# Kernel optimization log

Hardware: AMD Instinct MI355X
Metric: run time of the kernel (lower is better)

Reference implementation:

```python
import jax, jax.numpy as jnp
import numpy as np

B, L, HEADS, D_HEAD = 2, 2048, 16, 64
D_MODEL = HEADS * D_HEAD            # 1024
D_BI = D_MODEL * 4 // 2             # 2048 (bilinear GLU width)
D_PROJ = D_MODEL * 3 + 2 * D_BI
DEPTH = 0                           # block depth < 2 -> token shift active
NEG_INF = -1e10


def _ln(x, g, b, eps=1e-5):
    m = jnp.mean(x, axis=-1, keepdims=True)
    v = jnp.var(x, axis=-1, keepdims=True)
    return (x - m) * jax.lax.rsqrt(v + eps) * g + b


def _shift(x, n):
    # F.pad(x, (0,0,n,-n)): shift along seq dim by n, zero-fill at front
    return jnp.pad(x, ((0, 0), (n, 0), (0, 0)))[:, : x.shape[1], :]


def setup_inputs() -> dict:
    key = jax.random.key(0)
    ks = jax.random.split(key, 3)
    x = jax.random.normal(ks[0], (B, L, D_MODEL), jnp.float32)
    w_in = jax.random.normal(ks[1], (D_MODEL, D_PROJ), jnp.float32) * (D_MODEL ** -0.5)
    # note: torch init zeros out_proj; we use small random weights so backward is non-trivial
    w_out = jax.random.normal(ks[2], (D_MODEL + D_BI, D_MODEL), jnp.float32) * 0.02
    slopes = jnp.concatenate([2.0 ** jnp.linspace(0.0, -6.0, HEADS // 2),
                              jnp.zeros(HEADS - HEADS // 2)]).astype(jnp.float32)
    return {
        "x": x,
        "in_ln_g": jnp.ones(D_MODEL, jnp.float32), "in_ln_b": jnp.zeros(D_MODEL, jnp.float32),
        "mid_ln_g": jnp.ones(D_PROJ, jnp.float32), "mid_ln_b": jnp.zeros(D_PROJ, jnp.float32),
        "out_ln_g": jnp.ones(D_MODEL, jnp.float32), "out_ln_b": jnp.zeros(D_MODEL, jnp.float32),
        "w_in": w_in, "w_out": w_out, "slopes": slopes,
    }


def reference(x, in_ln_g, in_ln_b, mid_ln_g, mid_ln_b, out_ln_g, out_ln_b, w_in, w_out, slopes):
    b, l, d = x.shape
    x = _ln(x, in_ln_g, in_ln_b)
    if DEPTH < 2:
        x = jnp.concatenate([
            _shift(x[..., : d // 4], 1),
            x[..., d // 4: d - d // 8],
            _shift(x[..., d - d // 8:], 2),
        ], axis=-1)
    h = _ln(x @ w_in, mid_ln_g, mid_ln_b)
    q, k, v, p1, p2 = jnp.split(h, [D_MODEL, 2 * D_MODEL, 3 * D_MODEL, 3 * D_MODEL + D_BI], axis=-1)
    to_heads = lambda t: t.reshape(b, l, HEADS, D_HEAD).transpose(0, 2, 1, 3)  # b h l d
    q, k, v = to_heads(q), to_heads(k), to_heads(v)
    logits = jnp.einsum('bhid,bhjd->bhij', q, k) * (D_HEAD ** -0.5)
    pos = jnp.arange(l)
    alibi = pos[None, None, None, :].astype(logits.dtype) * slopes[None, :, None, None]
    causal = jnp.where(pos[:, None] >= pos[None, :], 0.0, NEG_INF).astype(logits.dtype)
    a = jax.nn.softmax(logits + alibi + causal, axis=-1)
    o = jnp.einsum('bhij,bhjd->bhid', a, v).transpose(0, 2, 1, 3).reshape(b, l, d)
    return _ln(jnp.concatenate([o, p1 * p2], axis=-1) @ w_out, out_ln_g, out_ln_b)
```

## Files before the change

kernel.cpp:

```cpp
#include <hip/hip_runtime.h>

#define B_ 2
#define L_ 2048
#define HEADS_ 16
#define DH_ 64
#define DM_ 1024
#define DBI_ 2048
#define DPROJ_ 7168
#define NTOK (B_*L_)
#define DCAT (DM_ + DBI_)

typedef __bf16 bf16;
typedef __attribute__((ext_vector_type(8))) __bf16 bf16x8;
typedef __attribute__((ext_vector_type(4))) __bf16 bf16x4;
typedef __attribute__((ext_vector_type(4))) float floatx4;

typedef __attribute__((address_space(1))) const void gptr_t;
typedef __attribute__((address_space(3))) void lptr_t;

__device__ __forceinline__ void g2l16(const void* g, void* l) {
    __builtin_amdgcn_global_load_lds((gptr_t*)g, (lptr_t*)l, 16, 0, 0);
}

__global__ __launch_bounds__(256) void transpose_both(const float* __restrict__ w_in,
                                                      const float* __restrict__ w_out,
                                                      bf16* __restrict__ w_inT,
                                                      bf16* __restrict__ w_outT) {
    __shared__ float tile[32][33];
    int l = blockIdx.x;
    const float* in; bf16* outp; int R, C, bx, by;
    if (l < 7168) { in = w_in;  outp = w_inT;  R = DM_;  C = DPROJ_; bx = l % 224; by = l / 224; }
    else { l -= 7168; in = w_out; outp = w_outT; R = DCAT; C = DM_;   bx = l % 32;  by = l / 32; }
    int c0 = bx * 32, r0 = by * 32;
    int x = threadIdx.x & 31, y = threadIdx.x >> 5;
    for (int i = 0; i < 32; i += 8)
        tile[y + i][x] = in[(size_t)(r0 + y + i) * C + (c0 + x)];
    __syncthreads();
    for (int i = 0; i < 32; i += 8)
        outp[(size_t)(c0 + y + i) * R + (r0 + x)] = (bf16)tile[x][y + i];
}

__global__ __launch_bounds__(256) void ln_shift(const float* __restrict__ x,
                                                const float* __restrict__ g,
                                                const float* __restrict__ bb,
                                                bf16* __restrict__ xs) {
    int tok = blockIdx.x;
    int b = tok / L_, l = tok % L_;
    int t = threadIdx.x;
    floatx4 v = *(const floatx4*)(x + (size_t)tok * DM_ + t * 4);
    float s = v[0] + v[1] + v[2] + v[3];
    float s2 = v[0]*v[0] + v[1]*v[1] + v[2]*v[2] + v[3]*v[3];
    __shared__ float red[2][4];
    for (int o = 32; o; o >>= 1) { s += __shfl_xor(s, o); s2 += __shfl_xor(s2, o); }
    int w = t >> 6;
    if ((t & 63) == 0) { red[0][w] = s; red[1][w] = s2; }
    __syncthreads();
    s  = red[0][0] + red[0][1] + red[0][2] + red[0][3];
    s2 = red[1][0] + red[1][1] + red[1][2] + red[1][3];
    float mean = s * (1.f / DM_);
    float var  = s2 * (1.f / DM_) - mean * mean;
    float rstd = rsqrtf(var + 1e-5f);
    int c0 = t * 4;
    floatx4 gg = *(const floatx4*)(g + c0);
    floatx4 bv = *(const floatx4*)(bb + c0);
    bf16x4 y;
    #pragma unroll
    for (int i = 0; i < 4; i++) y[i] = (bf16)((v[i] - mean) * rstd * gg[i] + bv[i]);
    int shift = (c0 < 256) ? 1 : ((c0 >= 896) ? 2 : 0);
    int dl = l + shift;
    if (dl < L_) *(bf16x4*)(xs + ((size_t)b * L_ + dl) * DM_ + c0) = y;
    if (l == 0 && shift) {
        bf16x4 z = {};
        *(bf16x4*)(xs + ((size_t)b * L_ + 0) * DM_ + c0) = z;
        if (shift == 2) *(bf16x4*)(xs + ((size_t)b * L_ + 1) * DM_ + c0) = z;
    }
}

__global__ __launch_bounds__(512, 2) void gemm1_fr(const bf16* __restrict__ A,
                                                   const bf16* __restrict__ Bt,
                                                   bf16* __restrict__ C) {
    const int K = DM_, N = DPROJ_;
    int lin = blockIdx.x;
    int xcd = lin & 7, idx = lin >> 3;
    int mt = (xcd >> 2) * 8 + idx / 7;
    int nt = (xcd & 3) * 7 + idx % 7;
    int m0 = mt * 256, n0 = nt * 256;

    __shared__ bf16 As[2][256 * 64];
    __shared__ bf16 Bs[2][256 * 64];

    int t = threadIdx.x;
    int lane = t & 63;
    int c = lane & 15, quad = lane >> 4;
    int wave = t >> 6;
    int wm = (wave >> 2) * 128;
    int wn = (wave & 3) * 64;

    auto stageA = [&](int k0, int bsel, int h) {
        #pragma unroll
        for (int s = 0; s < 2; s++) {
            int g = h * 1024 + s * 512 + t;
            int row = g >> 3;
            int kc = (g & 7) ^ (row & 7);
            g2l16(A + (size_t)(m0 + row) * K + (k0 + kc * 8), &As[bsel][g * 8]);
        }
    };
    auto stageB = [&](int k0, int bsel, int h) {
        #pragma unroll
        for (int s = 0; s < 2; s++) {
            int g = h * 1024 + s * 512 + t;
            int row = g >> 3;
            int kc = (g & 7) ^ (row & 7);
            g2l16(Bt + (size_t)(n0 + row) * K + (k0 + kc * 8), &Bs[bsel][g * 8]);
        }
    };

    floatx4 acc[8][4] = {};

    stageA(0, 0, 0); stageA(0, 0, 1);
    stageB(0, 0, 0); stageB(0, 0, 1);
    stageB(64, 1, 0); stageB(64, 1, 1);
    asm volatile("s_waitcnt vmcnt(4)" ::: "memory");
    __builtin_amdgcn_s_barrier();
    __builtin_amdgcn_sched_barrier(0);

    const int nT = K / 64;
    for (int tt = 0; tt < nT; ++tt) {
        int cur = tt & 1, nxt = cur ^ 1;
        int k1 = (tt + 1) << 6, k2 = (tt + 2) << 6;
        bool dA = (tt + 1 < nT), dB = (tt + 2 < nT);
        bf16x8 bfr[4][2];
        #pragma unroll
        for (int p = 0; p < 4; p++) {
            if      (p == 0) { if (dA) stageA(k1, nxt, 0); }
            else if (p == 1) { if (dA) stageA(k1, nxt, 1); }
            else if (p == 2) { if (dB) stageB(k2, cur, 0); }
            else             { if (dB) stageB(k2, cur, 1); }
            if (p == 0) {
                #pragma unroll
                for (int j = 0; j < 4; j++)
                    #pragma unroll
                    for (int s = 0; s < 2; s++)
                        bfr[j][s] = *(const bf16x8*)&Bs[cur][(wn + j * 16 + c) * 64
                                                            + (((s * 4 + quad) ^ (c & 7)) * 8)];
            }
            bf16x8 af[2][2];
            #pragma unroll
            for (int ii = 0; ii < 2; ii++)
                #pragma unroll
                for (int s = 0; s < 2; s++)
                    af[ii][s] = *(const bf16x8*)&As[cur][(wm + (p * 2 + ii) * 16 + c) * 64
                                                         + (((s * 4 + quad) ^ (c & 7)) * 8)];
            __builtin_amdgcn_s_setprio(1);
            #pragma unroll
            for (int ii = 0; ii < 2; ii++)
                #pragma unroll
                for (int j = 0; j < 4; j++)
                    #pragma unroll
                    for (int s = 0; s < 2; s++)
                        acc[p * 2 + ii][j] = __builtin_amdgcn_mfma_f32_16x16x32_bf16(
                            af[ii][s], bfr[j][s], acc[p * 2 + ii][j], 0, 0, 0);
            __builtin_amdgcn_s_setprio(0);
        }
        asm volatile("s_waitcnt lgkmcnt(0)" ::: "memory");
        if (dB)      { asm volatile("s_waitcnt vmcnt(4)" ::: "memory"); }
        else if (dA) { asm volatile("s_waitcnt vmcnt(0)" ::: "memory"); }
        if (tt + 1 < nT) __builtin_amdgcn_s_barrier();
        __builtin_amdgcn_sched_barrier(0);
    }

    #pragma unroll
    for (int i = 0; i < 8; i++)
        #pragma unroll
        for (int j = 0; j < 4; j++)
            #pragma unroll
            for (int r = 0; r < 4; r++) {
                int row = m0 + wm + i * 16 + quad * 4 + r;
                int col = n0 + wn + j * 16 + c;
                C[(size_t)row * N + col] = (bf16)acc[i][j][r];
            }
}

__global__ __launch_bounds__(256) void gemm2_sk(const bf16* __restrict__ A,
                                                const bf16* __restrict__ Bt,
                                                float* __restrict__ P) {
    const int ldA = DCAT, N = DM_;
    int m0 = blockIdx.x * 128, n0 = blockIdx.y * 128, kz = blockIdx.z;
    const bf16* Ak = A + kz * 1024;
    const bf16* Btk = Bt + kz * 1024;
    float* C = P + (size_t)kz * NTOK * DM_;
    __shared__ bf16 As[2][128 * 32];
    __shared__ bf16 Bs[2][128 * 32];
    int t = threadIdx.x, lane = t & 63, wave = t >> 6;
    int c = lane & 15, quad = lane >> 4;
    int wm = (wave >> 1) * 64, wn = (wave & 1) * 64;
    auto stage = [&](int k0, int bsel) {
        #pragma unroll
        for (int s = 0; s < 2; s++) {
            int f = s * 256 + t;
            int row = f >> 2, kp = (f & 3) * 8;
            g2l16(Ak + (size_t)(m0 + row) * ldA + k0 + kp, &As[bsel][f * 8]);
            g2l16(Btk + (size_t)(n0 + row) * ldA + k0 + kp, &Bs[bsel][f * 8]);
        }
    };
    floatx4 acc[4][4] = {};
    stage(0, 0);
    int buf = 0;
    for (int k0 = 0; k0 < 1024; k0 += 32) {
        __syncthreads();
        if (k0 + 32 < 1024) stage(k0 + 32, buf ^ 1);
        bf16x8 af[4], bfr[4];
        #pragma unroll
        for (int i = 0; i < 4; i++)
            af[i] = *(const bf16x8*)&As[buf][(wm + i * 16 + c) * 32 + quad * 8];
        #pragma unroll
        for (int j = 0; j < 4; j++)
            bfr[j] = *(const bf16x8*)&Bs[buf][(wn + j * 16 + c) * 32 + quad * 8];
        #pragma unroll
        for (int i = 0; i < 4; i++)
            #pragma unroll
            for (int j = 0; j < 4; j++)
                acc[i][j] = __builtin_amdgcn_mfma_f32_16x16x32_bf16(af[i], bfr[j], acc[i][j], 0, 0, 0);
        buf ^= 1;
    }
    #pragma unroll
    for (int i = 0; i < 4; i++)
        #pragma unroll
        for (int j = 0; j < 4; j++)
            #pragma unroll
            for (int r = 0; r < 4; r++) {
                int row = m0 + wm + i * 16 + quad * 4 + r;
                int col = n0 + wn + j * 16 + c;
                C[(size_t)row * N + col] = acc[i][j][r];
            }
}

__global__ __launch_bounds__(256) void mid_ln_fused(const bf16* __restrict__ h,
                                                    const float* __restrict__ g,
                                                    const float* __restrict__ bb,
                                                    bf16* __restrict__ Qp,
                                                    bf16* __restrict__ Kp,
                                                    bf16* __restrict__ Vn,
                                                    bf16* __restrict__ A2) {
    int tok = blockIdx.x;
    int b = tok >> 11, l = tok & 2047;
    size_t base = (size_t)tok * DPROJ_;
    int t = threadIdx.x;
    float v[28];
    float s = 0.f, s2 = 0.f;
    #pragma unroll
    for (int i = 0; i < 7; i++) {
        bf16x4 r = *(const bf16x4*)(h + base + (size_t)(t + i * 256) * 4);
        #pragma unroll
        for (int k = 0; k < 4; k++) {
            float f = (float)r[k];
            v[i * 4 + k] = f; s += f; s2 += f * f;
        }
    }
    __shared__ float red[2][4];
    for (int o = 32; o; o >>= 1) { s += __shfl_xor(s, o); s2 += __shfl_xor(s2, o); }
    int w = t >> 6;
    if ((t & 63) == 0) { red[0][w] = s; red[1][w] = s2; }
    __syncthreads();
    s  = red[0][0] + red[0][1] + red[0][2] + red[0][3];
    s2 = red[1][0] + red[1][1] + red[1][2] + red[1][3];
    float mean = s * (1.f / DPROJ_);
    float var  = s2 * (1.f / DPROJ_) - mean * mean;
    float rstd = rsqrtf(var + 1e-5f);
    #pragma unroll
    for (int i = 0; i < 7; i++) {
        int C0 = (t + i * 256) * 4;
        floatx4 gg = *(const floatx4*)(g + C0);
        floatx4 bv = *(const floatx4*)(bb + C0);
        #pragma unroll
        for (int k = 0; k < 4; k++)
            v[i * 4 + k] = (v[i * 4 + k] - mean) * rstd * gg[k] + bv[k];
    }
    #pragma unroll
    for (int i = 0; i < 3; i++) {
        int C0 = (t + i * 256) * 4;
        int sec = C0 >> 10, cc = C0 & 1023;
        int hh = cc >> 6, d = cc & 63;
        bf16* dst = (sec == 0) ? Qp : (sec == 1) ? Kp : Vn;
        size_t idx = (((size_t)b * HEADS_ + hh) * L_ + l) * DH_ + d;
        bf16x4 o;
        #pragma unroll
        for (int k = 0; k < 4; k++) o[k] = (bf16)v[i * 4 + k];
        *(bf16x4*)(dst + idx) = o;
    }
    #pragma unroll
    for (int i = 3; i < 5; i++) {
        int off = (t + i * 256) * 4 - 3 * DM_;
        bf16x4 o;
        #pragma unroll
        for (int k = 0; k < 4; k++) o[k] = (bf16)(v[i * 4 + k] * v[(i + 2) * 4 + k]);
        *(bf16x4*)(A2 + (size_t)tok * DCAT + DM_ + off) = o;
    }
}

__global__ __launch_bounds__(256) void vt_pack(const bf16* __restrict__ Vn,
                                               bf16* __restrict__ Vt) {
    __shared__ bf16 tile[32][33];
    int bh = blockIdx.z;
    const bf16* in = Vn + (size_t)bh * L_ * DH_;
    bf16* out = Vt + (size_t)bh * DH_ * L_;
    int l0 = blockIdx.x * 32, d0 = blockIdx.y * 32;
    int x = threadIdx.x & 31, y = threadIdx.x >> 5;
    for (int i = 0; i < 32; i += 8)
        tile[y + i][x] = in[(size_t)(l0 + y + i) * DH_ + d0 + x];
    __syncthreads();
    for (int i = 0; i < 32; i += 8)
        out[(size_t)(d0 + y + i) * L_ + l0 + x] = tile[x][y + i];
}

__global__ __launch_bounds__(256, 4) void attn6(const bf16* __restrict__ Qp,
                                                const bf16* __restrict__ Kp,
                                                const bf16* __restrict__ Vt,
                                                const float* __restrict__ slopes,
                                                bf16* __restrict__ A2) {
    int hd = blockIdx.y, b = blockIdx.z;
    int lin = blockIdx.x + 32 * blockIdx.y + 512 * blockIdx.z;
    int xr = blockIdx.x;
    int qt = ((lin >> 8) & 1) ? (31 - xr) : xr;
    int q0 = qt * 64;
    int t = threadIdx.x, lane = t & 63, wave = t >> 6;
    int quad = lane >> 4, c = lane & 15;
    __shared__ bf16 Ks[2][64 * 64];
    __shared__ bf16 Vs[64 * 64];
    __shared__ bf16 Ps[4][16 * 72];
    int bh = b * HEADS_ + hd;
    const bf16* Qb = Qp + (size_t)bh * L_ * DH_;
    const bf16* Kb = Kp + (size_t)bh * L_ * DH_;
    const bf16* Vb = Vt + (size_t)bh * DH_ * L_;
    const float LOG2E = 1.44269504f;
    float slopeL2 = slopes[hd] * LOG2E;
    const float qscale = 0.125f * LOG2E;

    bf16x8 qf[2];
    int qrow = q0 + wave * 16 + c;
    qf[0] = *(const bf16x8*)(Qb + (size_t)qrow * DH_ + quad * 8);
    qf[1] = *(const bf16x8*)(Qb + (size_t)qrow * DH_ + 32 + quad * 8);
    floatx4 accO[4] = {};
    float lsum[4];
    float mrow[4];
    int i_row0 = q0 + wave * 16 + quad * 4;
    #pragma unroll
    for (int r = 0; r < 4; r++) {
        lsum[r] = 0.f;
        mrow[r] = slopeL2 * (float)(i_row0 + r) + 20.0f;
    }

    int row = t >> 2, kp = (t & 3) * 8;
    auto stageK = [&](int j0, int kb) {
        #pragma unroll
        for (int s = 0; s < 2; s++)
            g2l16(Kb + (size_t)(j0 + row) * DH_ + s * 32 + kp, &Ks[kb][(s * 256 + t) * 8]);
    };
    auto stageV = [&](int j0) {
        #pragma unroll
        for (int s = 0; s < 2; s++)
            g2l16(Vb + (size_t)row * L_ + j0 + s * 32 + kp, &Vs[(s * 256 + t) * 8]);
    };

    bf16* pw = &Ps[wave][0];
    bf16* pwr = pw + (quad * 4) * 72 + c;

    stageK(0, 0);
    asm volatile("s_waitcnt vmcnt(0)" ::: "memory");
    __builtin_amdgcn_s_barrier();
    __builtin_amdgcn_sched_barrier(0);

    int kb = 0;
    for (int j0 = 0; j0 <= q0; j0 += 64) {
        bool dK = (j0 + 64 <= q0);
        stageV(j0);
        if (dK) stageK(j0 + 64, kb ^ 1);

        bool diag = (j0 == q0);
        #pragma unroll
        for (int nt = 0; nt < 4; nt++) {
            floatx4 sacc = {};
            bf16x8 kf0 = *(const bf16x8*)&Ks[kb][(nt * 16 + c) * 32 + quad * 8];
            bf16x8 kf1 = *(const bf16x8*)&Ks[kb][2048 + (nt * 16 + c) * 32 + quad * 8];
            sacc = __builtin_amdgcn_mfma_f32_16x16x32_bf16(qf[0], kf0, sacc, 0, 0, 0);
            sacc = __builtin_amdgcn_mfma_f32_16x16x32_bf16(qf[1], kf1, sacc, 0, 0, 0);
            int j = j0 + nt * 16 + c;
            float aj = slopeL2 * (float)j;
            #pragma unroll
            for (int r = 0; r < 4; r++) {
                float p = exp2f(fmaf(sacc[r], qscale, aj) - mrow[r]);
                if (diag) p = (j <= i_row0 + r) ? p : 0.f;
                lsum[r] += p;
                pwr[r * 72 + nt * 16] = (bf16)p;
            }
        }
        bf16x8 pf0 = *(const bf16x8*)&pw[c * 72 + quad * 8];
        bf16x8 pf1 = *(const bf16x8*)&pw[c * 72 + 32 + quad * 8];

        if (dK) { asm volatile("s_waitcnt vmcnt(2)" ::: "memory"); }
        else    { asm volatile("s_waitcnt vmcnt(0)" ::: "memory"); }
        __builtin_amdgcn_s_barrier();
        __builtin_amdgcn_sched_barrier(0);

        #pragma unroll
        for (int nt = 0; nt < 4; nt++) {
            bf16x8 vf0 = *(const bf16x8*)&Vs[(nt * 16 + c) * 32 + quad * 8];
            bf16x8 vf1 = *(const bf16x8*)&Vs[2048 + (nt * 16 + c) * 32 + quad * 8];
            accO[nt] = __builtin_amdgcn_mfma_f32_16x16x32_bf16(pf0, vf0, accO[nt], 0, 0, 0);
            accO[nt] = __builtin_amdgcn_mfma_f32_16x16x32_bf16(pf1, vf1, accO[nt], 0, 0, 0);
        }
        asm volatile("s_waitcnt lgkmcnt(0)" ::: "memory");
        __builtin_amdgcn_s_barrier();
        __builtin_amdgcn_sched_barrier(0);
        kb ^= 1;
    }
    #pragma unroll
    for (int r = 0; r < 4; r++) {
        float l = lsum[r];
        l += __shfl_xor(l, 1);
        l += __shfl_xor(l, 2);
        l += __shfl_xor(l, 4);
        l += __shfl_xor(l, 8);
        lsum[r] = 1.f / l;
    }
    #pragma unroll
    for (int r = 0; r < 4; r++) {
        size_t orow = (size_t)b * L_ + q0 + wave * 16 + quad * 4 + r;
        #pragma unroll
        for (int nt = 0; nt < 4; nt++)
            A2[orow * DCAT + hd * DH_ + nt * 16 + c] = (bf16)(accO[nt][r] * lsum[r]);
    }
}

__global__ __launch_bounds__(256) void out_ln3(const float* __restrict__ P,
                                               const float* __restrict__ g,
                                               const float* __restrict__ bb,
                                               float* __restrict__ out) {
    size_t base = (size_t)blockIdx.x * DM_;
    const size_t stride = (size_t)NTOK * DM_;
    int t = threadIdx.x;
    floatx4 a = *(const floatx4*)(P + base + t * 4);
    floatx4 b4 = *(const floatx4*)(P + base + stride + t * 4);
    floatx4 c4 = *(const floatx4*)(P + base + 2 * stride + t * 4);
    floatx4 v;
    #pragma unroll
    for (int i = 0; i < 4; i++) v[i] = a[i] + b4[i] + c4[i];
    float s = v[0] + v[1] + v[2] + v[3];
    float s2 = v[0]*v[0] + v[1]*v[1] + v[2]*v[2] + v[3]*v[3];
    __shared__ float red[2][4];
    for (int o = 32; o; o >>= 1) { s += __shfl_xor(s, o); s2 += __shfl_xor(s2, o); }
    int w = t >> 6;
    if ((t & 63) == 0) { red[0][w] = s; red[1][w] = s2; }
    __syncthreads();
    s  = red[0][0] + red[0][1] + red[0][2] + red[0][3];
    s2 = red[1][0] + red[1][1] + red[1][2] + red[1][3];
    float mean = s * (1.f / DM_);
    float var  = s2 * (1.f / DM_) - mean * mean;
    float rstd = rsqrtf(var + 1e-5f);
    int c0 = t * 4;
    floatx4 gg = *(const floatx4*)(g + c0);
    floatx4 bv = *(const floatx4*)(bb + c0);
    floatx4 o;
    #pragma unroll
    for (int i = 0; i < 4; i++) o[i] = (v[i] - mean) * rstd * gg[i] + bv[i];
    *(floatx4*)(out + base + c0) = o;
}

extern "C" void kernel_launch(void* const* d_in, const int* in_sizes, int n_in,
                              void* d_out, int out_size, void* d_ws, size_t ws_size,
                              hipStream_t stream) {
    const float* x     = (const float*)d_in[0];
    const float* in_g  = (const float*)d_in[1];
    const float* in_b  = (const float*)d_in[2];
    const float* mid_g = (const float*)d_in[3];
    const float* mid_b = (const float*)d_in[4];
    const float* out_g = (const float*)d_in[5];
    const float* out_b = (const float*)d_in[6];
    const float* w_in  = (const float*)d_in[7];
    const float* w_out = (const float*)d_in[8];
    const float* slopes = (const float*)d_in[9];
    float* out = (float*)d_out;

    char* ws = (char*)d_ws;
    size_t off = 0;
    auto alloc = [&](size_t n) { char* p = ws + off; off += (n + 255) & ~(size_t)255; return p; };
    bf16* w_inT  = (bf16*)alloc((size_t)DPROJ_ * DM_ * 2);
    bf16* w_outT = (bf16*)alloc((size_t)DM_ * DCAT * 2);
    bf16* xs     = (bf16*)alloc((size_t)NTOK * DM_ * 2);
    bf16* h      = (bf16*)alloc((size_t)NTOK * DPROJ_ * 2);
    bf16* A2     = (bf16*)alloc((size_t)NTOK * DCAT * 2);
    bf16* Qp     = (bf16*)alloc((size_t)NTOK * DM_ * 2);
    bf16* Kp     = (bf16*)alloc((size_t)NTOK * DM_ * 2);
    bf16* Vn     = (bf16*)alloc((size_t)NTOK * DM_ * 2);
    bf16* Vt = xs;
    float* P = (float*)h;

    hipLaunchKernelGGL(transpose_both, dim3(7168 + 3072), dim3(256), 0, stream,
                       w_in, w_out, w_inT, w_outT);
    hipLaunchKernelGGL(ln_shift, dim3(NTOK), dim3(256), 0, stream, x, in_g, in_b, xs);
    hipLaunchKernelGGL(gemm1_fr, dim3(448), dim3(512), 0, stream, xs, w_inT, h);
    hipLaunchKernelGGL(mid_ln_fused, dim3(NTOK), dim3(256), 0, stream, h, mid_g, mid_b,
                       Qp, Kp, Vn, A2);
    hipLaunchKernelGGL(vt_pack, dim3(L_ / 32, DH_ / 32, B_ * HEADS_), dim3(256), 0, stream, Vn, Vt);
    hipLaunchKernelGGL(attn6, dim3(32, HEADS_, B_), dim3(256), 0, stream, Qp, Kp, Vt, slopes, A2);
    hipLaunchKernelGGL(gemm2_sk, dim3(NTOK / 128, DM_ / 128, 3), dim3(256), 0, stream,
                       A2, w_outT, P);
    hipLaunchKernelGGL(out_ln3, dim3(NTOK), dim3(256), 0, stream, P, out_g, out_b, out);
}
```

Measured before the change: 304.5 us.

## Double attention query tile to 128 rows with 8-wave blocks sharing K/V tiles

```diff
diff --git a/kernel.cpp b/kernel.cpp
--- a/kernel.cpp
+++ b/kernel.cpp
@@ -313,21 +313,21 @@
         out[(size_t)(d0 + y + i) * L_ + l0 + x] = tile[x][y + i];
 }
 
-__global__ __launch_bounds__(256, 4) void attn6(const bf16* __restrict__ Qp,
+__global__ __launch_bounds__(512, 4) void attn7(const bf16* __restrict__ Qp,
                                                 const bf16* __restrict__ Kp,
                                                 const bf16* __restrict__ Vt,
                                                 const float* __restrict__ slopes,
                                                 bf16* __restrict__ A2) {
     int hd = blockIdx.y, b = blockIdx.z;
-    int lin = blockIdx.x + 32 * blockIdx.y + 512 * blockIdx.z;
+    int lin = blockIdx.x + 16 * blockIdx.y + 256 * blockIdx.z;
     int xr = blockIdx.x;
-    int qt = ((lin >> 8) & 1) ? (31 - xr) : xr;
-    int q0 = qt * 64;
+    int qt = ((lin >> 4) & 1) ? (15 - xr) : xr;
+    int q0 = qt * 128;
     int t = threadIdx.x, lane = t & 63, wave = t >> 6;
     int quad = lane >> 4, c = lane & 15;
     __shared__ bf16 Ks[2][64 * 64];
     __shared__ bf16 Vs[64 * 64];
-    __shared__ bf16 Ps[4][16 * 72];
+    __shared__ bf16 Ps[8][16 * 72];
     int bh = b * HEADS_ + hd;
     const bf16* Qb = Qp + (size_t)bh * L_ * DH_;
     const bf16* Kb = Kp + (size_t)bh * L_ * DH_;
@@ -350,16 +350,13 @@
         mrow[r] = slopeL2 * (float)(i_row0 + r) + 20.0f;
     }
 
-    int row = t >> 2, kp = (t & 3) * 8;
+    int sH = t >> 8, tt_ = t & 255;
+    int row = tt_ >> 2, kp = (tt_ & 3) * 8;
     auto stageK = [&](int j0, int kb) {
-        #pragma unroll
-        for (int s = 0; s < 2; s++)
-            g2l16(Kb + (size_t)(j0 + row) * DH_ + s * 32 + kp, &Ks[kb][(s * 256 + t) * 8]);
+        g2l16(Kb + (size_t)(j0 + row) * DH_ + sH * 32 + kp, &Ks[kb][t * 8]);
     };
     auto stageV = [&](int j0) {
-        #pragma unroll
-        for (int s = 0; s < 2; s++)
-            g2l16(Vb + (size_t)row * L_ + j0 + s * 32 + kp, &Vs[(s * 256 + t) * 8]);
+        g2l16(Vb + (size_t)row * L_ + j0 + sH * 32 + kp, &Vs[t * 8]);
     };
 
     bf16* pw = &Ps[wave][0];
@@ -371,43 +368,52 @@
     __builtin_amdgcn_sched_barrier(0);
 
     int kb = 0;
-    for (int j0 = 0; j0 <= q0; j0 += 64) {
-        bool dK = (j0 + 64 <= q0);
+    int jEnd = q0 + 64;
+    for (int j0 = 0; j0 <= jEnd; j0 += 64) {
+        bool dK = (j0 + 64 <= jEnd);
         stageV(j0);
         if (dK) stageK(j0 + 64, kb ^ 1);
 
-        bool diag = (j0 == q0);
-        #pragma unroll
-        for (int nt = 0; nt < 4; nt++) {
-            floatx4 sacc = {};
-            bf16x8 kf0 = *(const bf16x8*)&Ks[kb][(nt * 16 + c) * 32 + quad * 8];
-            bf16x8 kf1 = *(const bf16x8*)&Ks[kb][2048 + (nt * 16 + c) * 32 + quad * 8];
-            sacc = __builtin_amdgcn_mfma_f32_16x16x32_bf16(qf[0], kf0, sacc, 0, 0, 0);
-            sacc = __builtin_amdgcn_mfma_f32_16x16x32_bf16(qf[1], kf1, sacc, 0, 0, 0);
-            int j = j0 + nt * 16 + c;
-            float aj = slopeL2 * (float)j;
-            #pragma unroll
-            for (int r = 0; r < 4; r++) {
-                float p = exp2f(fmaf(sacc[r], qscale, aj) - mrow[r]);
-                if (diag) p = (j <= i_row0 + r) ? p : 0.f;
-                lsum[r] += p;
-                pwr[r * 72 + nt * 16] = (bf16)p;
+        bool active = (j0 <= q0 + wave * 16 + 15);
+        bool diag = (j0 + 63 > i_row0);
+        if (active) {
+            #pragma unroll
+            for (int nt = 0; nt < 4; nt++) {
+                floatx4 sacc = {};
+                bf16x8 kf0 = *(const bf16x8*)&Ks[kb][(nt * 16 + c) * 32 + quad * 8];
+                bf16x8 kf1 = *(const bf16x8*)&Ks[kb][2048 + (nt * 16 + c) * 32 + quad * 8];
+                sacc = __builtin_amdgcn_mfma_f32_16x16x32_bf16(qf[0], kf0, sacc, 0, 0, 0);
+                sacc = __builtin_amdgcn_mfma_f32_16x16x32_bf16(qf[1], kf1, sacc, 0, 0, 0);
+                int j = j0 + nt * 16 + c;
+                float aj = slopeL2 * (float)j;
+                #pragma unroll
+                for (int r = 0; r < 4; r++) {
+                    float p = exp2f(fmaf(sacc[r], qscale, aj) - mrow[r]);
+                    if (diag) p = (j <= i_row0 + r) ? p : 0.f;
+                    lsum[r] += p;
+                    pwr[r * 72 + nt * 16] = (bf16)p;
+                }
             }
         }
-        bf16x8 pf0 = *(const bf16x8*)&pw[c * 72 + quad * 8];
-        bf16x8 pf1 = *(const bf16x8*)&pw[c * 72 + 32 + quad * 8];
-
-        if (dK) { asm volatile("s_waitcnt vmcnt(2)" ::: "memory"); }
+        bf16x8 pf0, pf1;
+        if (active) {
+            pf0 = *(const bf16x8*)&pw[c * 72 + quad * 8];
+            pf1 = *(const bf16x8*)&pw[c * 72 + 32 + quad * 8];
+        }
+
+        if (dK) { asm volatile("s_waitcnt vmcnt(1)" ::: "memory"); }
         else    { asm volatile("s_waitcnt vmcnt(0)" ::: "memory"); }
         __builtin_amdgcn_s_barrier();
         __builtin_amdgcn_sched_barrier(0);
 
-        #pragma unroll
-        for (int nt = 0; nt < 4; nt++) {
-            bf16x8 vf0 = *(const bf16x8*)&Vs[(nt * 16 + c) * 32 + quad * 8];
-            bf16x8 vf1 = *(const bf16x8*)&Vs[2048 + (nt * 16 + c) * 32 + quad * 8];
-            accO[nt] = __builtin_amdgcn_mfma_f32_16x16x32_bf16(pf0, vf0, accO[nt], 0, 0, 0);
-            accO[nt] = __builtin_amdgcn_mfma_f32_16x16x32_bf16(pf1, vf1, accO[nt], 0, 0, 0);
+        if (active) {
+            #pragma unroll
+            for (int nt = 0; nt < 4; nt++) {
+                bf16x8 vf0 = *(const bf16x8*)&Vs[(nt * 16 + c) * 32 + quad * 8];
+                bf16x8 vf1 = *(const bf16x8*)&Vs[2048 + (nt * 16 + c) * 32 + quad * 8];
+                accO[nt] = __builtin_amdgcn_mfma_f32_16x16x32_bf16(pf0, vf0, accO[nt], 0, 0, 0);
+                accO[nt] = __builtin_amdgcn_mfma_f32_16x16x32_bf16(pf1, vf1, accO[nt], 0, 0, 0);
+            }
         }
         asm volatile("s_waitcnt lgkmcnt(0)" ::: "memory");
         __builtin_amdgcn_s_barrier();
@@ -502,7 +508,7 @@
     hipLaunchKernelGGL(mid_ln_fused, dim3(NTOK), dim3(256), 0, stream, h, mid_g, mid_b,
                        Qp, Kp, Vn, A2);
     hipLaunchKernelGGL(vt_pack, dim3(L_ / 32, DH_ / 32, B_ * HEADS_), dim3(256), 0, stream, Vn, Vt);
-    hipLaunchKernelGGL(attn6, dim3(32, HEADS_, B_), dim3(256), 0, stream, Qp, Kp, Vt, slopes, A2);
+    hipLaunchKernelGGL(attn7, dim3(16, HEADS_, B_), dim3(512), 0, stream, Qp, Kp, Vt, slopes, A2);
     hipLaunchKernelGGL(gemm2_sk, dim3(NTOK / 128, DM_ / 128, 3), dim3(256), 0, stream,
                        A2, w_outT, P);
     hipLaunchKernelGGL(out_ln3, dim3(NTOK), dim3(256), 0, stream, P, out_g, out_b, out);
```

After: 327.9 us. +7.7%, slower.
